# Optimization experiments

Hardware: AMD Instinct MI355X
Metric: run time of the kernel (lower is better)

The kernel has to match this reference:

```python
import jax, jax.numpy as jnp
import numpy as np
import math

B, S, DM, L = 4, 512, 768, 2
DI, DS, K = 2 * DM, 16, 4          # mamba_ssm defaults: expand=2, d_state=16, d_conv=4
DTR = math.ceil(DM / 16)           # dt_rank = 48
F = 1


def setup_inputs() -> dict:
    key = jax.random.key(0)
    ks = iter(jax.random.split(key, 16))
    g = lambda shape, s=0.02: jax.random.normal(next(ks), shape, jnp.float32) * s
    # sinusoidal positional encoding (precomputed buffer)
    pos = np.arange(S)[:, None].astype(np.float32)
    div = np.exp(np.arange(0, DM, 2).astype(np.float32) * (-math.log(10000.0) / DM))
    pe = np.zeros((S, DM), np.float32)
    pe[:, 0::2] = np.sin(pos * div)
    pe[:, 1::2] = np.cos(pos * div)
    # S4D-real style A init
    A_log = jnp.broadcast_to(jnp.log(jnp.arange(1, DS + 1, dtype=jnp.float32)), (L, DI, DS))
    return dict(
        x=jax.random.normal(next(ks), (B, S, F), jnp.float32),
        w_in=g((DM, F)), b_in=jnp.zeros((DM,), jnp.float32),
        pe=jnp.asarray(pe)[None],                       # (1, S, DM)
        ln1_w=jnp.ones((L, DM)), ln1_b=jnp.zeros((L, DM)),
        w_inproj=g((L, 2 * DI, DM)),
        conv_w=g((L, DI, K), 0.1), conv_b=jnp.zeros((L, DI)),
        w_xproj=g((L, DTR + 2 * DS, DI)),
        w_dt=g((L, DI, DTR)), b_dt=jnp.full((L, DI), -4.0, jnp.float32),
        A_log=A_log, D=jnp.ones((L, DI)),
        w_outproj=g((L, DM, DI)),
        ln2_w=jnp.ones((L, DM)), ln2_b=jnp.zeros((L, DM)),
        ff_w1=g((L, 2 * DM, DM)), ff_b1=jnp.zeros((L, 2 * DM)),
        ff_w2=g((L, DM, 2 * DM)), ff_b2=jnp.zeros((L, DM)),
        lnf_w=jnp.ones((DM,)), lnf_b=jnp.zeros((DM,)),
        w_head=g((1, DM)), b_head=jnp.zeros((1,), jnp.float32),
    )


def _ln(x, w, b):
    mu = x.mean(-1, keepdims=True)
    v = ((x - mu) ** 2).mean(-1, keepdims=True)
    return (x - mu) * jax.lax.rsqrt(v + 1e-5) * w + b


def _mamba(x, w_inproj, conv_w, conv_b, w_xproj, w_dt, b_dt, A_log, D_, w_outproj):
    # x: (B, S, DM)
    Bsz = x.shape[0]
    xz = jnp.einsum('bsd,ed->bse', x, w_inproj)         # (B, S, 2*DI)
    xm, z = jnp.split(xz, 2, axis=-1)
    # causal depthwise conv1d over time
    xc = jax.lax.conv_general_dilated(
        xm.transpose(0, 2, 1), conv_w[:, None, :], (1,), [(K - 1, 0)],
        feature_group_count=DI, dimension_numbers=('NCH', 'OIH', 'NCH'))
    xc = jax.nn.silu((xc + conv_b[:, None]).transpose(0, 2, 1))  # (B, S, DI)
    dbc = jnp.einsum('bsd,ed->bse', xc, w_xproj)        # (B, S, DTR+2*DS)
    dt, Bm, Cm = dbc[..., :DTR], dbc[..., DTR:DTR + DS], dbc[..., DTR + DS:]
    delta = jax.nn.softplus(jnp.einsum('bsr,dr->bsd', dt, w_dt) + b_dt)  # (B, S, DI)
    A = -jnp.exp(A_log)                                 # (DI, DS)

    def step(h, inp):
        d_t, B_t, C_t, u_t = inp                        # (B,DI),(B,DS),(B,DS),(B,DI)
        h = h * jnp.exp(d_t[:, :, None] * A) + (d_t * u_t)[:, :, None] * B_t[:, None, :]
        return h, jnp.einsum('bds,bs->bd', h, C_t)

    h0 = jnp.zeros((Bsz, DI, DS), x.dtype)
    _, ys = jax.lax.scan(step, h0, (delta.transpose(1, 0, 2), Bm.transpose(1, 0, 2),
                                    Cm.transpose(1, 0, 2), xc.transpose(1, 0, 2)))
    y = ys.transpose(1, 0, 2) + xc * D_
    y = y * jax.nn.silu(z)
    return jnp.einsum('bsd,ed->bse', y, w_outproj)


def reference(x, w_in, b_in, pe, ln1_w, ln1_b, w_inproj, conv_w, conv_b, w_xproj,
              w_dt, b_dt, A_log, D, w_outproj, ln2_w, ln2_b, ff_w1, ff_b1,
              ff_w2, ff_b2, lnf_w, lnf_b, w_head, b_head):
    h = jnp.einsum('bsf,df->bsd', x, w_in) + b_in
    h = h + pe[:, :h.shape[1]]
    for l in range(L):  # fixed small layer count
        h = h + _mamba(_ln(h, ln1_w[l], ln1_b[l]), w_inproj[l], conv_w[l], conv_b[l],
                       w_xproj[l], w_dt[l], b_dt[l], A_log[l], D[l], w_outproj[l])
        f = _ln(h, ln2_w[l], ln2_b[l])
        f = jax.nn.gelu(jnp.einsum('bsd,ed->bse', f, ff_w1[l]) + ff_b1[l], approximate=False)
        h = h + jnp.einsum('bse,de->bsd', f, ff_w2[l]) + ff_b2[l]
    h = _ln(h, lnf_w, lnf_b)
    h = h.mean(axis=1)                                  # mean pool over time
    return jnp.einsum('bd,od->bo', h, w_head) + b_head
```

## Files before the change

### kernel.cpp

```cpp
#include <hip/hip_runtime.h>
#include <hip/hip_bf16.h>
#include <math.h>

#define B_ 4
#define S_ 512
#define DM_ 768
#define L_ 2
#define DI_ 1536
#define DS_ 16
#define KC_ 4
#define DTR_ 48
#define NSEG 32
#define TS 16

typedef __hip_bfloat16 bf16;
typedef __attribute__((ext_vector_type(8))) short short8;
typedef __attribute__((ext_vector_type(4))) float f32x4;

#define GLDS16(g, l) __builtin_amdgcn_global_load_lds( \
    (const __attribute__((address_space(1))) void*)(g), \
    (__attribute__((address_space(3))) void*)(l), 16, 0, 0)


__global__ __launch_bounds__(256)
void k_embed_ln(const float* __restrict__ x, const float* __restrict__ w_in,
                const float* __restrict__ b_in, const float* __restrict__ pe,
                const float* __restrict__ lw, const float* __restrict__ lb,
                float* __restrict__ h, bf16* __restrict__ xout) {
  __shared__ float red1[4], red2[4];
  __shared__ float s_mu, s_rstd;
  int row = blockIdx.x;
  int s = row % S_;
  float xv = x[row];
  float v[3];
  float s1 = 0.f, s2 = 0.f;
#pragma unroll
  for (int j = 0; j < 3; ++j) {
    int d = threadIdx.x + j * 256;
    float t = xv * w_in[d] + b_in[d] + pe[s * DM_ + d];
    v[j] = t;
    s1 += t; s2 += t * t;
  }
  for (int off = 32; off; off >>= 1) { s1 += __shfl_down(s1, off); s2 += __shfl_down(s2, off); }
  if ((threadIdx.x & 63) == 0) { red1[threadIdx.x >> 6] = s1; red2[threadIdx.x >> 6] = s2; }
  __syncthreads();
  if (threadIdx.x == 0) {
    float t1 = red1[0] + red1[1] + red1[2] + red1[3];
    float t2 = red2[0] + red2[1] + red2[2] + red2[3];
    float mu = t1 * (1.f / DM_);
    float var = t2 * (1.f / DM_) - mu * mu;
    s_mu = mu;
    s_rstd = rsqrtf(var + 1e-5f);
  }
  __syncthreads();
  float mu = s_mu, rstd = s_rstd;
#pragma unroll
  for (int j = 0; j < 3; ++j) {
    int d = threadIdx.x + j * 256;
    h[(size_t)row * DM_ + d] = v[j];
    xout[(size_t)row * DM_ + d] = __float2bfloat16((v[j] - mu) * rstd * lw[d] + lb[d]);
  }
}

__global__ __launch_bounds__(256)
void k_lnred(const float* __restrict__ pxp, int KS,
             const float* __restrict__ hin, const float* __restrict__ bias,
             const float* __restrict__ lw, const float* __restrict__ lb,
             float* __restrict__ hout, bf16* __restrict__ xout) {
  __shared__ float red1[4], red2[4];
  __shared__ float s_mu, s_rstd;
  int row = blockIdx.x;
  float v[3];
  float s1 = 0.f, s2 = 0.f;
#pragma unroll
  for (int j = 0; j < 3; ++j) {
    int n = threadIdx.x + j * 256;
    float s = hin[(size_t)row * DM_ + n];
    if (bias) s += bias[n];
    for (int ks = 0; ks < KS; ++ks)
      s += pxp[(size_t)ks * 2048 * DM_ + (size_t)row * DM_ + n];
    v[j] = s;
    s1 += s; s2 += s * s;
  }
  for (int off = 32; off; off >>= 1) { s1 += __shfl_down(s1, off); s2 += __shfl_down(s2, off); }
  if ((threadIdx.x & 63) == 0) { red1[threadIdx.x >> 6] = s1; red2[threadIdx.x >> 6] = s2; }
  __syncthreads();
  if (threadIdx.x == 0) {
    float t1 = red1[0] + red1[1] + red1[2] + red1[3];
    float t2 = red2[0] + red2[1] + red2[2] + red2[3];
    float mu = t1 * (1.f / DM_);
    float var = t2 * (1.f / DM_) - mu * mu;
    s_mu = mu;
    s_rstd = rsqrtf(var + 1e-5f);
  }
  __syncthreads();
  float mu = s_mu, rstd = s_rstd;
#pragma unroll
  for (int j = 0; j < 3; ++j) {
    int n = threadIdx.x + j * 256;
    hout[(size_t)row * DM_ + n] = v[j];
    xout[(size_t)row * DM_ + n] = __float2bfloat16((v[j] - mu) * rstd * lw[n] + lb[n]);
  }
}

__global__ void k_gelred(const float* __restrict__ pxp, const float* __restrict__ bias,
                         bf16* __restrict__ out) {
  int idx = blockIdx.x * 256 + threadIdx.x;
  if (idx >= 2048 * 2 * DM_) return;
  int n = idx % (2 * DM_);
  float s = pxp[idx] + pxp[(size_t)2048 * 2 * DM_ + idx] + bias[n];
  s = 0.5f * s * (1.f + erff(s * 0.70710678118654752f));
  out[idx] = __float2bfloat16(s);
}

typedef struct { unsigned short x, y, z, w; } us4;
__device__ __forceinline__ void cast4(const float* __restrict__ s, bf16* __restrict__ d) {
  float4 v = *(const float4*)s;
  us4 o;
  o.x = __bfloat16_as_ushort(__float2bfloat16(v.x));
  o.y = __bfloat16_as_ushort(__float2bfloat16(v.y));
  o.z = __bfloat16_as_ushort(__float2bfloat16(v.z));
  o.w = __bfloat16_as_ushort(__float2bfloat16(v.w));
  *(us4*)d = o;
}
__device__ __forceinline__ void store4(bf16* __restrict__ d, float a, float b, float c, float e) {
  us4 o;
  o.x = __bfloat16_as_ushort(__float2bfloat16(a));
  o.y = __bfloat16_as_ushort(__float2bfloat16(b));
  o.z = __bfloat16_as_ushort(__float2bfloat16(c));
  o.w = __bfloat16_as_ushort(__float2bfloat16(e));
  *(us4*)d = o;
}

__global__ void k_castall(const float* __restrict__ w_inproj, const float* __restrict__ w_outproj,
                          const float* __restrict__ ff_w1, const float* __restrict__ ff_w2,
                          const float* __restrict__ w_xproj, const float* __restrict__ w_dt,
                          const float* __restrict__ A_log,
                          bf16* __restrict__ wip, bf16* __restrict__ wop,
                          bf16* __restrict__ wf1, bf16* __restrict__ wf2,
                          bf16* __restrict__ wxp, bf16* __restrict__ wdtp,
                          float* __restrict__ At) {
  const int N0 = L_ * 2 * DI_ * DM_;
  const int N1 = L_ * DM_ * DI_;
  const int N2 = L_ * 2 * DM_ * DM_;
  const int N3 = L_ * DM_ * 2 * DM_;
  const int N4 = L_ * 128 * DI_;
  const int N5 = L_ * DI_ * 64;
  const int N6 = L_ * 16 * DI_;
  const int T4 = (N0 + N1 + N2 + N3 + N4 + N5) >> 2;
  int tid = blockIdx.x * 256 + threadIdx.x;
  int stride = gridDim.x * 256;
  for (int v = tid; v < T4; v += stride) {
    int j = v << 2;
    if (j < N0) { cast4(w_inproj + j, wip + j); continue; }
    j -= N0;
    if (j < N1) { cast4(w_outproj + j, wop + j); continue; }
    j -= N1;
    if (j < N2) { cast4(ff_w1 + j, wf1 + j); continue; }
    j -= N2;
    if (j < N3) { cast4(ff_w2 + j, wf2 + j); continue; }
    j -= N3;
    if (j < N4) {
      int col = j % DI_;
      int row = (j / DI_) & 127;
      int l = j / (128 * DI_);
      if (row < 80) cast4(&w_xproj[((size_t)l * 80 + row) * DI_ + col], wxp + j);
      else store4(wxp + j, 0.f, 0.f, 0.f, 0.f);
      continue;
    }
    j -= N4;
    {
      int col = j & 63;
      int r = (j >> 6) % DI_;
      int l = j / (DI_ * 64);
      if (col < 48) cast4(&w_dt[((size_t)l * DI_ + r) * 48 + col], wdtp + j);
      else store4(wdtp + j, 0.f, 0.f, 0.f, 0.f);
    }
  }
  for (int j = tid; j < N6; j += stride) {
    int d = j % DI_;
    int n = (j / DI_) & 15;
    int l = j / (16 * DI_);
    At[j] = -__expf(A_log[((size_t)l * DI_ + d) * 16 + n]);
  }
}

__global__ void k_conv_silu(const bf16* __restrict__ xz, const float* __restrict__ cw,
                            const float* __restrict__ cb, float* __restrict__ xc,
                            bf16* __restrict__ xcb) {
  int idx = blockIdx.x * 256 + threadIdx.x;
  if (idx >= B_ * S_ * DI_) return;
  int d = idx % DI_;
  int t = idx / DI_;
  int s = t % S_;
  int b = t / S_;
  float acc = cb[d];
  const bf16* base = xz + (size_t)(b * S_) * (2 * DI_) + d;
#pragma unroll
  for (int k = 0; k < KC_; ++k) {
    int ss = s - (KC_ - 1) + k;
    if (ss >= 0) acc = fmaf(__bfloat162float(base[(size_t)ss * (2 * DI_)]), cw[d * KC_ + k], acc);
  }
  float v = acc / (1.f + expf(-acc));
  xc[idx] = v;
  xcb[idx] = __float2bfloat16(v);
}

__global__ __launch_bounds__(256)
void k_scanA(const float* __restrict__ delta, const float* __restrict__ xc,
             const float* __restrict__ bc, const float* __restrict__ At,
             const float* __restrict__ Dv,
             float* __restrict__ ylocal, float* __restrict__ cumd,
             float* __restrict__ hend) {
  int b = blockIdx.y;
  int seg = blockIdx.z;
  int d = blockIdx.x * 256 + threadIdx.x;
  int s0 = seg * TS;

  float A[16], hst[16];
#pragma unroll
  for (int n = 0; n < 16; ++n) {
    A[n] = At[(size_t)n * DI_ + d];
    hst[n] = 0.f;
  }
  float Dd = Dv[d];
  float cd = 0.f;

  const float* dp = delta + ((size_t)(b * S_ + s0)) * DI_ + d;
  const float* up = xc + ((size_t)(b * S_ + s0)) * DI_ + d;
  const float* bp = bc + ((size_t)(b * S_ + s0)) * 32;
  float* yp = ylocal + ((size_t)(b * S_ + s0)) * DI_ + d;
  float* cp = cumd + ((size_t)(b * S_ + s0)) * DI_ + d;

  float dl_next = dp[0];
  float u_next = up[0];
#pragma unroll 4
  for (int s = 0; s < TS; ++s) {
    float dl = dl_next, u = u_next;
    if (s + 1 < TS) {
      dl_next = dp[(size_t)(s + 1) * DI_];
      u_next = up[(size_t)(s + 1) * DI_];
    }
    cd += dl;
    float dlu = dl * u;
    float y = 0.f;
#pragma unroll
    for (int n = 0; n < 16; ++n) {
      float e = __expf(dl * A[n]);
      hst[n] = fmaf(hst[n], e, dlu * bp[s * 32 + n]);
      y = fmaf(hst[n], bp[s * 32 + 16 + n], y);
    }
    yp[(size_t)s * DI_] = fmaf(u, Dd, y);
    cp[(size_t)s * DI_] = cd;
  }
  float* hp = hend + ((size_t)(b * NSEG + seg) * 16) * DI_ + d;
#pragma unroll
  for (int n = 0; n < 16; ++n) hp[(size_t)n * DI_] = hst[n];
}

__global__ void k_scanB(const float* __restrict__ hend, const float* __restrict__ cumd,
                        const float* __restrict__ At, float* __restrict__ h0seg) {
  int idx = blockIdx.x * 256 + threadIdx.x;
  if (idx >= B_ * 16 * DI_) return;
  int d = idx % DI_;
  int r = idx / DI_;
  int n = r & 15;
  int b = r >> 4;
  float A = At[(size_t)n * DI_ + d];
  float h0 = 0.f;
  for (int seg = 0; seg < NSEG; ++seg) {
    size_t o = ((size_t)(b * NSEG + seg) * 16 + n) * DI_ + d;
    h0seg[o] = h0;
    float cdt = cumd[((size_t)(b * S_ + seg * TS + TS - 1)) * DI_ + d];
    h0 = h0 * __expf(A * cdt) + hend[o];
  }
}

__global__ __launch_bounds__(256)
void k_scanC(const float* __restrict__ ylocal, const float* __restrict__ cumd,
             const float* __restrict__ bc, const float* __restrict__ At,
             const float* __restrict__ h0seg, const bf16* __restrict__ xz,
             bf16* __restrict__ yb16) {
  int d = blockIdx.x * 256 + threadIdx.x;
  int t = blockIdx.y;
  int b = blockIdx.z;
  int seg = t / TS;
  size_t o = ((size_t)(b * S_ + t)) * DI_ + d;
  float y = ylocal[o];
  if (seg) {
    float cd = cumd[o];
    const float* Cp = bc + ((size_t)(b * S_ + t)) * 32 + 16;
    const float* Hb = h0seg + ((size_t)(b * NSEG + seg) * 16) * DI_ + d;
#pragma unroll
    for (int n = 0; n < 16; ++n)
      y += Cp[n] * __expf(At[(size_t)n * DI_ + d] * cd) * Hb[(size_t)n * DI_];
  }
  float z = __bfloat162float(xz[((size_t)(b * S_ + t)) * (2 * DI_) + DI_ + d]);
  float sig = 1.f / (1.f + __expf(-z));
  yb16[o] = __float2bfloat16(y * (z * sig));
}

__global__ void k_head1(const bf16* __restrict__ hf, const float* __restrict__ wh,
                        float* __restrict__ partial) {
  __shared__ float red[4];
  int b = blockIdx.y, j = blockIdx.x;
  const bf16* base = hf + ((size_t)b * S_ + j * 32) * DM_;
  float acc = 0.f;
  for (int i = threadIdx.x; i < 32 * DM_; i += 256) {
    int dd = i - (i / DM_) * DM_;
    acc += __bfloat162float(base[i]) * wh[dd];
  }
  for (int off = 32; off; off >>= 1) acc += __shfl_down(acc, off);
  if ((threadIdx.x & 63) == 0) red[threadIdx.x >> 6] = acc;
  __syncthreads();
  if (threadIdx.x == 0)
    partial[b * 16 + j] = red[0] + red[1] + red[2] + red[3];
}

__global__ void k_head2(const float* __restrict__ partial, const float* __restrict__ bh,
                        float* __restrict__ out) {
  int b = threadIdx.x;
  if (b < B_) {
    float acc = 0.f;
    for (int j = 0; j < 16; ++j) acc += partial[b * 16 + j];
    out[b] = acc * (1.f / S_) + bh[0];
  }
}

template <int EPI>
__global__ __launch_bounds__(256)
void k_gemm_mfma(const bf16* __restrict__ A, int lda,
                 const bf16* __restrict__ W, int ldw,
                 const float* __restrict__ bias,
                 void* __restrict__ out1,
                 int ldc, int N, int Kdim, int pmn) {
  __shared__ short As[2][8192];
  __shared__ short Bs[2][8192];

  int nwg = gridDim.x * gridDim.y;
  int orig = blockIdx.y * gridDim.x + blockIdx.x;
  int wg = (nwg % 8 == 0) ? ((orig & 7) * (nwg >> 3) + (orig >> 3)) : orig;
  int m0 = (wg / gridDim.x) * 128;
  int n0 = (wg % gridDim.x) * 128;

  int lane = threadIdx.x & 63;
  int wid = threadIdx.x >> 6;
  int wm = wid >> 1, wn = wid & 1;
  int lr = lane & 15;
  int ch = lane >> 4;
  int koff = blockIdx.z * Kdim;

  f32x4 acc[4][4];
#pragma unroll
  for (int i = 0; i < 4; ++i)
#pragma unroll
    for (int j = 0; j < 4; ++j) {
      acc[i][j][0] = 0.f; acc[i][j][1] = 0.f; acc[i][j][2] = 0.f; acc[i][j][3] = 0.f;
    }

#define GSTAGE(bb, kt)                                                            \
  {                                                                               \
    int k0 = koff + (kt) * 64;                                                    \
    _Pragma("unroll")                                                             \
    for (int c0 = 0; c0 < 4; ++c0) {                                              \
      int c = c0 * 256 + (int)threadIdx.x;                                        \
      int row = c & 127, chk = c >> 7;                                            \
      GLDS16(A + (size_t)(m0 + row) * lda + k0 + chk * 8,                         \
             (char*)&As[bb][0] + c * 16);                                         \
      GLDS16(W + (size_t)(n0 + row) * ldw + k0 + chk * 8,                         \
             (char*)&Bs[bb][0] + c * 16);                                         \
    }                                                                             \
  }

  int nt = Kdim / 64;
  GSTAGE(0, 0);

  for (int t = 0; t < nt; ++t) {
    int buf = t & 1;
    if (t + 1 < nt) {
      GSTAGE(buf ^ 1, t + 1);
      asm volatile("s_waitcnt vmcnt(8)" ::: "memory");
    } else {
      asm volatile("s_waitcnt vmcnt(0)" ::: "memory");
    }
    __builtin_amdgcn_s_barrier();
    __builtin_amdgcn_sched_barrier(0);

    short8 a0[4], a1[4], b0[4], b1[4];
#pragma unroll
    for (int f = 0; f < 4; ++f) {
      a0[f] = *(const short8*)&As[buf][(ch * 128 + wm * 64 + f * 16 + lr) * 8];
      b0[f] = *(const short8*)&Bs[buf][(ch * 128 + wn * 64 + f * 16 + lr) * 8];
    }
    __builtin_amdgcn_sched_barrier(0);
#pragma unroll
    for (int f = 0; f < 4; ++f) {
      a1[f] = *(const short8*)&As[buf][((4 + ch) * 128 + wm * 64 + f * 16 + lr) * 8];
      b1[f] = *(const short8*)&Bs[buf][((4 + ch) * 128 + wn * 64 + f * 16 + lr) * 8];
    }
    asm volatile("s_waitcnt lgkmcnt(8)" ::: "memory");
    __builtin_amdgcn_sched_barrier(0);
    __builtin_amdgcn_s_setprio(1);
#pragma unroll
    for (int i = 0; i < 4; ++i)
#pragma unroll
      for (int j = 0; j < 4; ++j)
        acc[i][j] = __builtin_amdgcn_mfma_f32_16x16x32_bf16(a0[i], b0[j], acc[i][j], 0, 0, 0);
    __builtin_amdgcn_sched_barrier(0);
    asm volatile("s_waitcnt lgkmcnt(0)" ::: "memory");
    __builtin_amdgcn_sched_barrier(0);
#pragma unroll
    for (int i = 0; i < 4; ++i)
#pragma unroll
      for (int j = 0; j < 4; ++j)
        acc[i][j] = __builtin_amdgcn_mfma_f32_16x16x32_bf16(a1[i], b1[j], acc[i][j], 0, 0, 0);
    __builtin_amdgcn_s_setprio(0);
    __builtin_amdgcn_sched_barrier(0);
    __builtin_amdgcn_s_barrier();
  }
#undef GSTAGE

#pragma unroll
  for (int i = 0; i < 4; ++i) {
#pragma unroll
    for (int j = 0; j < 4; ++j) {
      int nl = wn * 64 + j * 16 + (lane & 15);
      int n = n0 + nl;
#pragma unroll
      for (int q = 0; q < 4; ++q) {
        int m = m0 + wm * 64 + i * 16 + (lane >> 4) * 4 + q;
        float v = acc[i][j][q];
        if (EPI == 0) {
          ((float*)out1)[(size_t)m * ldc + n] = v;
        } else if (EPI == 3) {
          v += bias[n];
          v = (v > 20.f) ? v : log1pf(expf(v));
          ((float*)out1)[(size_t)m * ldc + n] = v;
        } else if (EPI == 5) {
          ((float*)out1)[(size_t)blockIdx.z * pmn + (size_t)m * N + n] = v;
        } else if (EPI == 6) {
          ((bf16*)out1)[(size_t)m * ldc + n] = __float2bfloat16(v);
        }
      }
    }
  }
}

__global__ void k_xreduce(const float* __restrict__ pxp, bf16* __restrict__ dtp,
                          float* __restrict__ bcb) {
  int idx = blockIdx.x * 256 + threadIdx.x;
  if (idx >= 2048 * 128) return;
  int m = idx >> 7, n = idx & 127;
  float s = 0.f;
#pragma unroll
  for (int k = 0; k < 8; ++k) s += pxp[(size_t)k * 2048 * 128 + idx];
  if (n < 64) dtp[m * 64 + n] = __float2bfloat16(n < 48 ? s : 0.f);
  if (n >= 48 && n < 80) bcb[m * 32 + (n - 48)] = s;
}


extern "C" void kernel_launch(void* const* d_in, const int* in_sizes, int n_in,
                              void* d_out, int out_size, void* d_ws, size_t ws_size,
                              hipStream_t stream) {
  const float* x        = (const float*)d_in[0];
  const float* w_in     = (const float*)d_in[1];
  const float* b_in     = (const float*)d_in[2];
  const float* pe       = (const float*)d_in[3];
  const float* ln1_w    = (const float*)d_in[4];
  const float* ln1_b    = (const float*)d_in[5];
  const float* w_inproj = (const float*)d_in[6];
  const float* conv_w   = (const float*)d_in[7];
  const float* conv_b   = (const float*)d_in[8];
  const float* w_xproj  = (const float*)d_in[9];
  const float* w_dt     = (const float*)d_in[10];
  const float* b_dt     = (const float*)d_in[11];
  const float* A_log    = (const float*)d_in[12];
  const float* Dv       = (const float*)d_in[13];
  const float* w_outproj= (const float*)d_in[14];
  const float* ln2_w    = (const float*)d_in[15];
  const float* ln2_b    = (const float*)d_in[16];
  const float* ff_w1    = (const float*)d_in[17];
  const float* ff_b1    = (const float*)d_in[18];
  const float* ff_w2    = (const float*)d_in[19];
  const float* ff_b2    = (const float*)d_in[20];
  const float* lnf_w    = (const float*)d_in[21];
  const float* lnf_b    = (const float*)d_in[22];
  const float* w_head   = (const float*)d_in[23];
  const float* b_head   = (const float*)d_in[24];
  float* out = (float*)d_out;

  const int M = B_ * S_;

  float* wsf = (float*)d_ws;
  float* h    = wsf; wsf += (size_t)M * DM_;
  float* xc   = wsf; wsf += (size_t)M * DI_;
  float* bc   = wsf; wsf += (size_t)M * 32;
  float* dlt  = wsf; wsf += (size_t)M * DI_;
  float* hend = wsf; wsf += (size_t)B_ * NSEG * DI_ * 16;
  float* h0sg = wsf; wsf += (size_t)B_ * NSEG * DI_ * 16;
  float* pxp  = wsf; wsf += (size_t)4 * M * 2 * DM_;
  float* At   = wsf; wsf += (size_t)L_ * 16 * DI_;
  float* part = wsf; wsf += 64;
  bf16* wsb = (bf16*)wsf;
  bf16* xln16 = wsb; wsb += (size_t)M * DM_;
  bf16* xz16  = wsb; wsb += (size_t)M * 2 * DI_;
  bf16* xcb   = wsb; wsb += (size_t)M * DI_;
  bf16* dtp   = wsb; wsb += (size_t)M * 64;
  bf16* yb16  = wsb; wsb += (size_t)M * DI_;
  bf16* ffh16 = wsb; wsb += (size_t)M * DI_;
  bf16* wip   = wsb; wsb += (size_t)L_ * 2 * DI_ * DM_;
  bf16* wxp   = wsb; wsb += (size_t)L_ * 128 * DI_;
  bf16* wdtp  = wsb; wsb += (size_t)L_ * DI_ * 64;
  bf16* wop   = wsb; wsb += (size_t)L_ * DM_ * DI_;
  bf16* wf1   = wsb; wsb += (size_t)L_ * 2 * DM_ * DM_;
  bf16* wf2   = wsb; wsb += (size_t)L_ * DM_ * 2 * DM_;

  float* ylocal = dlt;
  float* cumd   = xc;

  dim3 blk(256);

  k_castall<<<1024, blk, 0, stream>>>(w_inproj, w_outproj, ff_w1, ff_w2,
                                      w_xproj, w_dt, A_log,
                                      wip, wop, wf1, wf2, wxp, wdtp, At);

  k_embed_ln<<<M, blk, 0, stream>>>(x, w_in, b_in, pe, ln1_w, ln1_b, h, xln16);

  for (int l = 0; l < L_; ++l) {
    const float* Atl = At + (size_t)l * 16 * DI_;

    k_gemm_mfma<6><<<dim3(2 * DI_ / 128, M / 128), blk, 0, stream>>>(
        xln16, DM_, wip + (size_t)l * 2 * DI_ * DM_, DM_, nullptr,
        xz16, 2 * DI_, 2 * DI_, DM_, 0);

    k_conv_silu<<<(B_ * S_ * DI_ + 255) / 256, blk, 0, stream>>>(
        xz16, conv_w + l * DI_ * KC_, conv_b + l * DI_, xc, xcb);

    k_gemm_mfma<5><<<dim3(1, M / 128, 8), blk, 0, stream>>>(
        xcb, DI_, wxp + (size_t)l * 128 * DI_, DI_, nullptr,
        pxp, 128, 128, DI_ / 8, M * 128);
    k_xreduce<<<(M * 128) / 256, blk, 0, stream>>>(pxp, dtp, bc);

    k_gemm_mfma<3><<<dim3(DI_ / 128, M / 128), blk, 0, stream>>>(
        dtp, 64, wdtp + (size_t)l * DI_ * 64, 64, b_dt + l * DI_,
        dlt, DI_, DI_, 64, 0);

    k_scanA<<<dim3(DI_ / 256, B_, NSEG), blk, 0, stream>>>(
        dlt, xc, bc, Atl, Dv + l * DI_, ylocal, cumd, hend);
    k_scanB<<<(B_ * 16 * DI_ + 255) / 256, blk, 0, stream>>>(hend, cumd, Atl, h0sg);
    k_scanC<<<dim3(DI_ / 256, S_, B_), blk, 0, stream>>>(
        ylocal, cumd, bc, Atl, h0sg, xz16, yb16);

    k_gemm_mfma<5><<<dim3(DM_ / 128, M / 128, 4), blk, 0, stream>>>(
        yb16, DI_, wop + (size_t)l * DM_ * DI_, DI_, nullptr,
        pxp, DM_, DM_, DI_ / 4, M * DM_);
    k_lnred<<<M, blk, 0, stream>>>(pxp, 4, h, nullptr,
                                   ln2_w + l * DM_, ln2_b + l * DM_, h, xln16);

    k_gemm_mfma<5><<<dim3(2 * DM_ / 128, M / 128, 2), blk, 0, stream>>>(
        xln16, DM_, wf1 + (size_t)l * 2 * DM_ * DM_, DM_, nullptr,
        pxp, 2 * DM_, 2 * DM_, DM_ / 2, M * 2 * DM_);
    k_gelred<<<(M * 2 * DM_) / 256, blk, 0, stream>>>(pxp, ff_b1 + l * 2 * DM_, ffh16);

    k_gemm_mfma<5><<<dim3(DM_ / 128, M / 128, 4), blk, 0, stream>>>(
        ffh16, 2 * DM_, wf2 + (size_t)l * DM_ * 2 * DM_, 2 * DM_, nullptr,
        pxp, DM_, DM_, DI_ / 4, M * DM_);
    const float* nlw = (l + 1 < L_) ? ln1_w + (l + 1) * DM_ : lnf_w;
    const float* nlb = (l + 1 < L_) ? ln1_b + (l + 1) * DM_ : lnf_b;
    k_lnred<<<M, blk, 0, stream>>>(pxp, 4, h, ff_b2 + l * DM_, nlw, nlb, h, xln16);
  }

  k_head1<<<dim3(16, B_), blk, 0, stream>>>(xln16, w_head, part);
  k_head2<<<1, 64, 0, stream>>>(part, b_head, out);
}
```

Baseline: 492.1 us.

## Cut fp32 intermediates: bf16 FF1 partials, drop fp32 conv output, merge head kernels

Several independent traffic cuts. The FF1 split-K partials are now stored in bf16 through a new GEMM epilogue and summed in the GELU reduce. The conv kernel writes only the bf16 output and handles two channels per thread, with the scan reading bf16 u. The two head kernels become a single 1024-thread kernel per batch. Storing partials and u in bf16 loses precision in exchange for less memory traffic, and the head now runs on only four blocks.

New measurement: 607.4 us. 1.23x slower.

```diff
diff --git a/kernel.cpp b/kernel.cpp
--- a/kernel.cpp
+++ b/kernel.cpp
@@ -103,12 +103,13 @@
   }
 }
 
-__global__ void k_gelred(const float* __restrict__ pxp, const float* __restrict__ bias,
+__global__ void k_gelred(const bf16* __restrict__ pxp, const float* __restrict__ bias,
                          bf16* __restrict__ out) {
   int idx = blockIdx.x * 256 + threadIdx.x;
   if (idx >= 2048 * 2 * DM_) return;
   int n = idx % (2 * DM_);
-  float s = pxp[idx] + pxp[(size_t)2048 * 2 * DM_ + idx] + bias[n];
+  float s = __bfloat162float(pxp[idx]) +
+            __bfloat162float(pxp[(size_t)2048 * 2 * DM_ + idx]) + bias[n];
   s = 0.5f * s * (1.f + erff(s * 0.70710678118654752f));
   out[idx] = __float2bfloat16(s);
 }
@@ -123,12 +124,8 @@
   o.w = __bfloat16_as_ushort(__float2bfloat16(v.w));
   *(us4*)d = o;
 }
-__device__ __forceinline__ void store4(bf16* __restrict__ d, float a, float b, float c, float e) {
-  us4 o;
-  o.x = __bfloat16_as_ushort(__float2bfloat16(a));
-  o.y = __bfloat16_as_ushort(__float2bfloat16(b));
-  o.z = __bfloat16_as_ushort(__float2bfloat16(c));
-  o.w = __bfloat16_as_ushort(__float2bfloat16(e));
+__device__ __forceinline__ void store4z(bf16* __restrict__ d) {
+  us4 o; o.x = o.y = o.z = o.w = 0;
   *(us4*)d = o;
 }
 
@@ -165,7 +162,7 @@
       int row = (j / DI_) & 127;
       int l = j / (128 * DI_);
       if (row < 80) cast4(&w_xproj[((size_t)l * 80 + row) * DI_ + col], wxp + j);
-      else store4(wxp + j, 0.f, 0.f, 0.f, 0.f);
+      else store4z(wxp + j);
       continue;
     }
     j -= N4;
@@ -174,7 +171,7 @@
       int r = (j >> 6) % DI_;
       int l = j / (DI_ * 64);
       if (col < 48) cast4(&w_dt[((size_t)l * DI_ + r) * 48 + col], wdtp + j);
-      else store4(wdtp + j, 0.f, 0.f, 0.f, 0.f);
+      else store4z(wdtp + j);
     }
   }
   for (int j = tid; j < N6; j += stride) {
@@ -186,28 +183,35 @@
 }
 
 __global__ void k_conv_silu(const bf16* __restrict__ xz, const float* __restrict__ cw,
-                            const float* __restrict__ cb, float* __restrict__ xc,
-                            bf16* __restrict__ xcb) {
+                            const float* __restrict__ cb, bf16* __restrict__ xcb) {
   int idx = blockIdx.x * 256 + threadIdx.x;
-  if (idx >= B_ * S_ * DI_) return;
-  int d = idx % DI_;
-  int t = idx / DI_;
+  if (idx >= B_ * S_ * (DI_ / 2)) return;
+  int d2 = idx % (DI_ / 2);
+  int d = d2 * 2;
+  int t = idx / (DI_ / 2);
   int s = t % S_;
   int b = t / S_;
-  float acc = cb[d];
+  float a0 = cb[d], a1 = cb[d + 1];
   const bf16* base = xz + (size_t)(b * S_) * (2 * DI_) + d;
 #pragma unroll
   for (int k = 0; k < KC_; ++k) {
     int ss = s - (KC_ - 1) + k;
-    if (ss >= 0) acc = fmaf(__bfloat162float(base[(size_t)ss * (2 * DI_)]), cw[d * KC_ + k], acc);
-  }
-  float v = acc / (1.f + expf(-acc));
-  xc[idx] = v;
-  xcb[idx] = __float2bfloat16(v);
+    if (ss >= 0) {
+      ushort2 v = *(const ushort2*)&base[(size_t)ss * (2 * DI_)];
+      a0 = fmaf(__bfloat162float(__ushort_as_bfloat16(v.x)), cw[d * KC_ + k], a0);
+      a1 = fmaf(__bfloat162float(__ushort_as_bfloat16(v.y)), cw[(d + 1) * KC_ + k], a1);
+    }
+  }
+  float v0 = a0 / (1.f + expf(-a0));
+  float v1 = a1 / (1.f + expf(-a1));
+  ushort2 o;
+  o.x = __bfloat16_as_ushort(__float2bfloat16(v0));
+  o.y = __bfloat16_as_ushort(__float2bfloat16(v1));
+  *(ushort2*)&xcb[(size_t)t * DI_ + d] = o;
 }
 
 __global__ __launch_bounds__(256)
-void k_scanA(const float* __restrict__ delta, const float* __restrict__ xc,
+void k_scanA(const float* __restrict__ delta, const bf16* __restrict__ xcb,
              const float* __restrict__ bc, const float* __restrict__ At,
              const float* __restrict__ Dv,
              float* __restrict__ ylocal, float* __restrict__ cumd,
@@ -227,19 +231,19 @@
   float cd = 0.f;
 
   const float* dp = delta + ((size_t)(b * S_ + s0)) * DI_ + d;
-  const float* up = xc + ((size_t)(b * S_ + s0)) * DI_ + d;
+  const bf16* up = xcb + ((size_t)(b * S_ + s0)) * DI_ + d;
   const float* bp = bc + ((size_t)(b * S_ + s0)) * 32;
   float* yp = ylocal + ((size_t)(b * S_ + s0)) * DI_ + d;
   float* cp = cumd + ((size_t)(b * S_ + s0)) * DI_ + d;
 
   float dl_next = dp[0];
-  float u_next = up[0];
+  float u_next = __bfloat162float(up[0]);
 #pragma unroll 4
   for (int s = 0; s < TS; ++s) {
     float dl = dl_next, u = u_next;
     if (s + 1 < TS) {
       dl_next = dp[(size_t)(s + 1) * DI_];
-      u_next = up[(size_t)(s + 1) * DI_];
+      u_next = __bfloat162float(up[(size_t)(s + 1) * DI_]);
     }
     cd += dl;
     float dlu = dl * u;
@@ -300,30 +304,23 @@
   yb16[o] = __float2bfloat16(y * (z * sig));
 }
 
-__global__ void k_head1(const bf16* __restrict__ hf, const float* __restrict__ wh,
-                        float* __restrict__ partial) {
-  __shared__ float red[4];
-  int b = blockIdx.y, j = blockIdx.x;
-  const bf16* base = hf + ((size_t)b * S_ + j * 32) * DM_;
+__global__ __launch_bounds__(1024)
+void k_head(const bf16* __restrict__ hf, const float* __restrict__ wh,
+            const float* __restrict__ bh, float* __restrict__ out) {
+  __shared__ float red[16];
+  int b = blockIdx.x;
+  const bf16* base = hf + (size_t)b * S_ * DM_;
   float acc = 0.f;
-  for (int i = threadIdx.x; i < 32 * DM_; i += 256) {
-    int dd = i - (i / DM_) * DM_;
-    acc += __bfloat162float(base[i]) * wh[dd];
-  }
+  for (int i = threadIdx.x; i < S_ * DM_; i += 1024)
+    acc += __bfloat162float(base[i]) * wh[i % DM_];
   for (int off = 32; off; off >>= 1) acc += __shfl_down(acc, off);
   if ((threadIdx.x & 63) == 0) red[threadIdx.x >> 6] = acc;
   __syncthreads();
-  if (threadIdx.x == 0)
-    partial[b * 16 + j] = red[0] + red[1] + red[2] + red[3];
-}
-
-__global__ void k_head2(const float* __restrict__ partial, const float* __restrict__ bh,
-                        float* __restrict__ out) {
-  int b = threadIdx.x;
-  if (b < B_) {
-    float acc = 0.f;
-    for (int j = 0; j < 16; ++j) acc += partial[b * 16 + j];
-    out[b] = acc * (1.f / S_) + bh[0];
+  if (threadIdx.x == 0) {
+    float t = 0.f;
+#pragma unroll
+    for (int j = 0; j < 16; ++j) t += red[j];
+    out[b] = t * (1.f / S_) + bh[0];
   }
 }
 
@@ -440,6 +437,8 @@
           ((float*)out1)[(size_t)blockIdx.z * pmn + (size_t)m * N + n] = v;
         } else if (EPI == 6) {
           ((bf16*)out1)[(size_t)m * ldc + n] = __float2bfloat16(v);
+        } else if (EPI == 7) {
+          ((bf16*)out1)[(size_t)blockIdx.z * pmn + (size_t)m * N + n] = __float2bfloat16(v);
         }
       }
     }
@@ -493,14 +492,13 @@
 
   float* wsf = (float*)d_ws;
   float* h    = wsf; wsf += (size_t)M * DM_;
-  float* xc   = wsf; wsf += (size_t)M * DI_;
   float* bc   = wsf; wsf += (size_t)M * 32;
   float* dlt  = wsf; wsf += (size_t)M * DI_;
+  float* cumd = wsf; wsf += (size_t)M * DI_;
   float* hend = wsf; wsf += (size_t)B_ * NSEG * DI_ * 16;
   float* h0sg = wsf; wsf += (size_t)B_ * NSEG * DI_ * 16;
   float* pxp  = wsf; wsf += (size_t)4 * M * 2 * DM_;
   float* At   = wsf; wsf += (size_t)L_ * 16 * DI_;
-  float* part = wsf; wsf += 64;
   bf16* wsb = (bf16*)wsf;
   bf16* xln16 = wsb; wsb += (size_t)M * DM_;
   bf16* xz16  = wsb; wsb += (size_t)M * 2 * DI_;
@@ -516,7 +514,7 @@
   bf16* wf2   = wsb; wsb += (size_t)L_ * DM_ * 2 * DM_;
 
   float* ylocal = dlt;
-  float* cumd   = xc;
+  bf16* pxp16 = (bf16*)pxp;
 
   dim3 blk(256);
 
@@ -533,8 +531,8 @@
         xln16, DM_, wip + (size_t)l * 2 * DI_ * DM_, DM_, nullptr,
         xz16, 2 * DI_, 2 * DI_, DM_, 0);
 
-    k_conv_silu<<<(B_ * S_ * DI_ + 255) / 256, blk, 0, stream>>>(
-        xz16, conv_w + l * DI_ * KC_, conv_b + l * DI_, xc, xcb);
+    k_conv_silu<<<(B_ * S_ * (DI_ / 2) + 255) / 256, blk, 0, stream>>>(
+        xz16, conv_w + l * DI_ * KC_, conv_b + l * DI_, xcb);
 
     k_gemm_mfma<5><<<dim3(1, M / 128, 8), blk, 0, stream>>>(
         xcb, DI_, wxp + (size_t)l * 128 * DI_, DI_, nullptr,
@@ -546,7 +544,7 @@
         dlt, DI_, DI_, 64, 0);
 
     k_scanA<<<dim3(DI_ / 256, B_, NSEG), blk, 0, stream>>>(
-        dlt, xc, bc, Atl, Dv + l * DI_, ylocal, cumd, hend);
+        dlt, xcb, bc, Atl, Dv + l * DI_, ylocal, cumd, hend);
     k_scanB<<<(B_ * 16 * DI_ + 255) / 256, blk, 0, stream>>>(hend, cumd, Atl, h0sg);
     k_scanC<<<dim3(DI_ / 256, S_, B_), blk, 0, stream>>>(
         ylocal, cumd, bc, Atl, h0sg, xz16, yb16);
@@ -557,10 +555,10 @@
     k_lnred<<<M, blk, 0, stream>>>(pxp, 4, h, nullptr,
                                    ln2_w + l * DM_, ln2_b + l * DM_, h, xln16);
 
-    k_gemm_mfma<5><<<dim3(2 * DM_ / 128, M / 128, 2), blk, 0, stream>>>(
+    k_gemm_mfma<7><<<dim3(2 * DM_ / 128, M / 128, 2), blk, 0, stream>>>(
         xln16, DM_, wf1 + (size_t)l * 2 * DM_ * DM_, DM_, nullptr,
-        pxp, 2 * DM_, 2 * DM_, DM_ / 2, M * 2 * DM_);
-    k_gelred<<<(M * 2 * DM_) / 256, blk, 0, stream>>>(pxp, ff_b1 + l * 2 * DM_, ffh16);
+        pxp16, 2 * DM_, 2 * DM_, DM_ / 2, M * 2 * DM_);
+    k_gelred<<<(M * 2 * DM_) / 256, blk, 0, stream>>>(pxp16, ff_b1 + l * 2 * DM_, ffh16);
 
     k_gemm_mfma<5><<<dim3(DM_ / 128, M / 128, 4), blk, 0, stream>>>(
         ffh16, 2 * DM_, wf2 + (size_t)l * DM_ * 2 * DM_, 2 * DM_, nullptr,
@@ -570,6 +568,5 @@
     k_lnred<<<M, blk, 0, stream>>>(pxp, 4, h, ff_b2 + l * DM_, nlw, nlb, h, xln16);
   }
 
-  k_head1<<<dim3(16, B_), blk, 0, stream>>>(xln16, w_head, part);
-  k_head2<<<1, 64, 0, stream>>>(part, b_head, out);
-}
+  k_head<<<B_, 1024, 0, stream>>>(xln16, w_head, b_head, out);
+}
```
